# Kernel tuning notes

Hardware: AMD Instinct MI355X
Metric: run time of the kernel (lower is better)

The kernel has to match this reference:

```python
import jax, jax.numpy as jnp
import numpy as np

BLOCK_SIZE = 32
EPS = 1e-6


def setup_inputs() -> dict:
    key = jax.random.key(0)
    k1, k2, k3, k4, k5 = jax.random.split(key, 5)
    B, H, L, D = 2, 16, 4096, 128
    return {
        "query_states": jax.random.normal(k1, (B, H, L, D), dtype=jnp.float32),
        "key_states": jax.random.normal(k2, (B, H, L, D), dtype=jnp.float32),
        "value_states": jax.random.normal(k3, (B, H, L, D), dtype=jnp.float32),
        # learned params; init near torch defaults (ones/zeros) with small noise
        "phi_scale": 1.0 + 0.1 * jax.random.normal(k4, (H, 1, D), dtype=jnp.float32),
        "phi_bias": 0.1 * jax.random.normal(k5, (H, 1, D), dtype=jnp.float32),
    }


def _forward(query_states, key_states, value_states, phi_scale, phi_bias):
    B, H, L, D = query_states.shape
    bs = BLOCK_SIZE
    N = L // bs  # L chosen divisible by block_size (no padding path)

    def feature_map(x):  # x: (B,H,N,bs,D)
        # phi_scale (H,1,D) -> (H,1,1,D) broadcasts over (B,H,N,bs,D)
        y = jax.nn.elu(x * phi_scale[:, None] + phi_bias[:, None]) + 1.0
        return jnp.clip(y, 0.0, 10.0)

    q = query_states.reshape(B, H, N, bs, D)
    k = key_states.reshape(B, H, N, bs, D)
    v = value_states.reshape(B, H, N, bs, D)

    phi_q = feature_map(q)
    phi_k = feature_map(k)

    # move block axis to front for scan: (N,B,H,bs,D)
    pq = jnp.moveaxis(phi_q, 2, 0)
    pk = jnp.moveaxis(phi_k, 2, 0)
    vb = jnp.moveaxis(v, 2, 0)

    S0 = jnp.zeros((B, H, D, D), dtype=jnp.float32)
    Z0 = jnp.zeros((B, H, D), dtype=jnp.float32)

    def step(carry, inp):
        S, Z = carry
        pq_n, pk_n, v_n = inp  # each (B,H,bs,D)
        # block-causal, bidirectional within block: update state BEFORE output
        S = S + jnp.einsum('bhkd,bhke->bhde', pk_n, v_n)
        Z = Z + pk_n.sum(axis=-2)
        num = jnp.einsum('bhqd,bhde->bhqe', pq_n, S)
        den = jnp.maximum(jnp.einsum('bhqd,bhd->bhq', pq_n, Z), EPS)
        return (S, Z), num / den[..., None]

    _, out_blocks = jax.lax.scan(step, (S0, Z0), (pq, pk, vb))  # (N,B,H,bs,D)
    out = jnp.moveaxis(out_blocks, 0, 2).reshape(B, H, L, D)
    return out


def reference(query_states, key_states, value_states, phi_scale, phi_bias):
    return _forward(query_states, key_states, value_states, phi_scale, phi_bias)
```

## Files before the change

kernel.cpp:

```cpp
#include <hip/hip_runtime.h>
#include <stdint.h>

#define BH 32
#define LSEQ 4096
#define DDIM 128
#define BS 32
#define NBLK 128
#define CHUNKS 16
#define BLK_PER_CHUNK 8
#define STATE_SZ (DDIM*DDIM + DDIM)

typedef __attribute__((ext_vector_type(8))) short bf16x8;
typedef __attribute__((ext_vector_type(4))) float f32x4;

__device__ inline uint16_t f2bf(float f) {
    uint32_t x = __builtin_bit_cast(uint32_t, f);
    x += 0x7fffu + ((x >> 16) & 1u);
    return (uint16_t)(x >> 16);
}
__device__ inline float bflo(uint32_t w){ return __builtin_bit_cast(float, w << 16); }
__device__ inline float bfhi(uint32_t w){ return __builtin_bit_cast(float, w & 0xffff0000u); }

__device__ inline float phi_f(float x, float s, float b) {
    float y = fmaf(x, s, b);
    float pos = fminf(y + 1.0f, 10.0f);
    float neg = __expf(y);
    return (y > 0.0f) ? pos : neg;
}

#define SMEM_BYTES 62080

template<bool PHASE2>
__global__ __launch_bounds__(512, 4) void la_phase(
    const float* __restrict__ Q, const float* __restrict__ K,
    const float* __restrict__ V, const float* __restrict__ scale,
    const float* __restrict__ bias, float* __restrict__ states,
    float* __restrict__ out)
{
    extern __shared__ char smem[];
    uint16_t* S_bfT  = (uint16_t*)smem;
    uint16_t* pk_bf  = (uint16_t*)smem;
    uint16_t* v_bf   = (uint16_t*)(smem + 8704);
    uint16_t* pkT    = (uint16_t*)(smem + 34816);
    uint16_t* pq_bf  = pkT;
    uint16_t* vT     = (uint16_t*)(smem + 45056);
    float* Zl        = (float*)(smem + 55296);
    float* Zpart     = Zl + 128;
    float* den_part  = Zpart + 8*128;
    float* inv_den   = den_part + 32*16;

    const int tid  = threadIdx.x;
    const int bid  = blockIdx.x;
    const int bh   = bid >> 4;
    const int ch   = bid & 15;
    const int lane = tid & 63;
    const int wv   = tid >> 6;
    const int i15  = lane & 15;
    const int q4   = lane >> 4;

    const size_t base = (size_t)bh * LSEQ * DDIM;
    const int h = bh & 15;

    const int sr = tid >> 4;
    const int sc = (tid & 15) * 8;

    float sreg[8], breg[8];
    #pragma unroll
    for (int j = 0; j < 8; ++j) {
        sreg[j] = scale[h*DDIM + sc + j];
        breg[j] = bias[h*DDIM + sc + j];
    }

    f32x4 accS[8];
    float* stbase = states + (size_t)(bh*CHUNKS + ch) * STATE_SZ;

    if (PHASE2) {
        #pragma unroll
        for (int mt = 0; mt < 8; ++mt) {
            #pragma unroll
            for (int r = 0; r < 4; ++r) {
                int d = 16*mt + 4*q4 + r;
                accS[mt][r] = stbase[d*DDIM + 16*wv + i15];
            }
        }
        if (tid < 128) Zl[tid] = stbase[DDIM*DDIM + tid];
    } else {
        #pragma unroll
        for (int mt = 0; mt < 8; ++mt) accS[mt] = (f32x4){0.f,0.f,0.f,0.f};
        if (tid < 128) Zl[tid] = 0.f;
    }
    __syncthreads();

    for (int s = 0; s < BLK_PER_CHUNK; ++s) {
        const int blk = ch * BLK_PER_CHUNK + s;
        const size_t rowoff = base + (size_t)(blk*BS + sr) * DDIM + sc;

        {
            const float4 k0 = *(const float4*)(K + rowoff);
            const float4 k1 = *(const float4*)(K + rowoff + 4);
            const float4 v0 = *(const float4*)(V + rowoff);
            const float4 v1 = *(const float4*)(V + rowoff + 4);
            float kp[8] = {k0.x,k0.y,k0.z,k0.w,k1.x,k1.y,k1.z,k1.w};
            float vp[8] = {v0.x,v0.y,v0.z,v0.w,v1.x,v1.y,v1.z,v1.w};
            uint32_t pk[4], pv[4];
            #pragma unroll
            for (int j = 0; j < 4; ++j) {
                uint32_t lo = f2bf(phi_f(kp[2*j],   sreg[2*j],   breg[2*j]));
                uint32_t hi = f2bf(phi_f(kp[2*j+1], sreg[2*j+1], breg[2*j+1]));
                pk[j] = lo | (hi << 16);
                lo = f2bf(vp[2*j]); hi = f2bf(vp[2*j+1]);
                pv[j] = lo | (hi << 16);
            }
            *(uint4*)&pk_bf[sr*136 + sc] = *(uint4*)pk;
            *(uint4*)&v_bf [sr*136 + sc] = *(uint4*)pv;
        }
        __syncthreads();

        {
            const int dp  = tid & 63;
            const int seg = tid >> 6;
            const int r0  = seg * 4;
            uint32_t w0 = *(const uint32_t*)&pk_bf[(r0+0)*136 + 2*dp];
            uint32_t w1 = *(const uint32_t*)&pk_bf[(r0+1)*136 + 2*dp];
            uint32_t w2 = *(const uint32_t*)&pk_bf[(r0+2)*136 + 2*dp];
            uint32_t w3 = *(const uint32_t*)&pk_bf[(r0+3)*136 + 2*dp];
            uint2 lo, hi;
            lo.x = (w0 & 0xffffu) | (w1 << 16);
            lo.y = (w2 & 0xffffu) | (w3 << 16);
            hi.x = (w0 >> 16) | (w1 & 0xffff0000u);
            hi.y = (w2 >> 16) | (w3 & 0xffff0000u);
            *(uint2*)&pkT[(2*dp+0)*40 + r0] = lo;
            *(uint2*)&pkT[(2*dp+1)*40 + r0] = hi;
            Zpart[seg*128 + 2*dp+0] = bflo(w0)+bflo(w1)+bflo(w2)+bflo(w3);
            Zpart[seg*128 + 2*dp+1] = bfhi(w0)+bfhi(w1)+bfhi(w2)+bfhi(w3);
            w0 = *(const uint32_t*)&v_bf[(r0+0)*136 + 2*dp];
            w1 = *(const uint32_t*)&v_bf[(r0+1)*136 + 2*dp];
            w2 = *(const uint32_t*)&v_bf[(r0+2)*136 + 2*dp];
            w3 = *(const uint32_t*)&v_bf[(r0+3)*136 + 2*dp];
            lo.x = (w0 & 0xffffu) | (w1 << 16);
            lo.y = (w2 & 0xffffu) | (w3 << 16);
            hi.x = (w0 >> 16) | (w1 & 0xffff0000u);
            hi.y = (w2 >> 16) | (w3 & 0xffff0000u);
            *(uint2*)&vT[(2*dp+0)*40 + r0] = lo;
            *(uint2*)&vT[(2*dp+1)*40 + r0] = hi;
        }
        __syncthreads();

        if (tid < 128) {
            float z = Zl[tid];
            #pragma unroll
            for (int g = 0; g < 8; ++g) z += Zpart[g*128 + tid];
            Zl[tid] = z;
        }
        {
            bf16x8 bv = *(const bf16x8*)&vT[(16*wv + i15)*40 + 8*q4];
            #pragma unroll
            for (int mt = 0; mt < 8; ++mt) {
                bf16x8 av = *(const bf16x8*)&pkT[(16*mt + i15)*40 + 8*q4];
                accS[mt] = __builtin_amdgcn_mfma_f32_16x16x32_bf16(av, bv, accS[mt], 0, 0, 0);
            }
        }

        if (PHASE2) {
            __syncthreads();

            {
                const float4 a0 = *(const float4*)(Q + rowoff);
                const float4 a1 = *(const float4*)(Q + rowoff + 4);
                float qp[8] = {a0.x,a0.y,a0.z,a0.w,a1.x,a1.y,a1.z,a1.w};
                uint32_t pq[4];
                #pragma unroll
                for (int j = 0; j < 4; ++j) {
                    uint32_t lo = f2bf(phi_f(qp[2*j],   sreg[2*j],   breg[2*j]));
                    uint32_t hi = f2bf(phi_f(qp[2*j+1], sreg[2*j+1], breg[2*j+1]));
                    pq[j] = lo | (hi << 16);
                }
                *(uint4*)&pq_bf[sr*136 + sc] = *(uint4*)pq;
            }
            #pragma unroll
            for (int mt = 0; mt < 8; ++mt) {
                uint2 o;
                o.x = (uint32_t)f2bf(accS[mt][0]) | ((uint32_t)f2bf(accS[mt][1]) << 16);
                o.y = (uint32_t)f2bf(accS[mt][2]) | ((uint32_t)f2bf(accS[mt][3]) << 16);
                *(uint2*)&S_bfT[(16*wv + i15)*136 + 16*mt + 4*q4] = o;
            }
            __syncthreads();

            f32x4 acc2[2];
            acc2[0] = (f32x4){0.f,0.f,0.f,0.f};
            acc2[1] = (f32x4){0.f,0.f,0.f,0.f};
            #pragma unroll
            for (int ks = 0; ks < 4; ++ks) {
                bf16x8 sb = *(const bf16x8*)&S_bfT[(16*wv + i15)*136 + 32*ks + 8*q4];
                #pragma unroll
                for (int qt = 0; qt < 2; ++qt) {
                    bf16x8 qa = *(const bf16x8*)&pq_bf[(16*qt + i15)*136 + 32*ks + 8*q4];
                    acc2[qt] = __builtin_amdgcn_mfma_f32_16x16x32_bf16(qa, sb, acc2[qt], 0, 0, 0);
                }
            }
            {
                const int dq = tid >> 4;
                const int pt = tid & 15;
                float sden = 0.f;
                #pragma unroll
                for (int j = 0; j < 4; ++j) {
                    uint32_t w = *(const uint32_t*)&pq_bf[dq*136 + 8*pt + 2*j];
                    sden += bflo(w) * Zl[8*pt + 2*j] + bfhi(w) * Zl[8*pt + 2*j + 1];
                }
                den_part[dq*16 + pt] = sden;
            }
            __syncthreads();
            if (tid < 32) {
                float sden = 0.f;
                #pragma unroll
                for (int j = 0; j < 16; ++j) sden += den_part[tid*16 + j];
                inv_den[tid] = 1.0f / fmaxf(sden, 1e-6f);
            }
            __syncthreads();

            #pragma unroll
            for (int qt = 0; qt < 2; ++qt) {
                #pragma unroll
                for (int r = 0; r < 4; ++r) {
                    int qrow = 16*qt + 4*q4 + r;
                    float o = acc2[qt][r] * inv_den[qrow];
                    out[base + (size_t)(blk*BS + qrow)*DDIM + 16*wv + i15] = o;
                }
            }
        }
    }

    if (!PHASE2) {
        #pragma unroll
        for (int mt = 0; mt < 8; ++mt) {
            #pragma unroll
            for (int r = 0; r < 4; ++r) {
                int d = 16*mt + 4*q4 + r;
                stbase[d*DDIM + 16*wv + i15] = accS[mt][r];
            }
        }
        if (tid < 128) stbase[DDIM*DDIM + tid] = Zl[tid];
    }
}

__global__ void la_prefix(float* __restrict__ states) {
    const int bh = blockIdx.x >> 4;
    const int sl = blockIdx.x & 15;
    const int slice = STATE_SZ / 16;
    float* p0 = states + (size_t)bh * CHUNKS * STATE_SZ + sl * slice;
    for (int i = threadIdx.x; i < slice; i += 256) {
        float run = 0.f;
        float* p = p0 + i;
        #pragma unroll
        for (int c = 0; c < CHUNKS; ++c) {
            float v = p[(size_t)c * STATE_SZ];
            p[(size_t)c * STATE_SZ] = run;
            run += v;
        }
    }
}

extern "C" void kernel_launch(void* const* d_in, const int* in_sizes, int n_in,
                              void* d_out, int out_size, void* d_ws, size_t ws_size,
                              hipStream_t stream) {
    const float* Q     = (const float*)d_in[0];
    const float* K     = (const float*)d_in[1];
    const float* V     = (const float*)d_in[2];
    const float* scale = (const float*)d_in[3];
    const float* bias  = (const float*)d_in[4];
    float* out    = (float*)d_out;
    float* states = (float*)d_ws;

    hipLaunchKernelGGL((la_phase<false>), dim3(BH*CHUNKS), dim3(512), SMEM_BYTES, stream,
                       Q, K, V, scale, bias, states, out);
    hipLaunchKernelGGL(la_prefix, dim3(BH*16), dim3(256), 0, stream, states);
    hipLaunchKernelGGL((la_phase<true>), dim3(BH*CHUNKS), dim3(512), SMEM_BYTES, stream,
                       Q, K, V, scale, bias, states, out);
}
```

Before: 269.5 us.

## Pipeline chunk loop with register prefetch, shuffle transpose, and swizzled LDS

Restructures the per-chunk loop so the next block's K/V/Q loads are issued into registers while the current block's MFMAs run. The pk/v transpose moves from an LDS round-trip to wave shuffles, LDS tiles get XOR-style swizzles against bank conflicts, and the denominator reduction uses shuffles instead of a shared partial array. Several barriers per iteration are removed, and output stores are deferred by one iteration. The state save/load is made coalesced, and the prefix-sum kernel runs one thread per element with all loads hoisted. The cost is higher register pressure and more complex index logic.

```diff
diff --git a/kernel.cpp b/kernel.cpp
--- a/kernel.cpp
+++ b/kernel.cpp
@@ -1,22 +1,21 @@
 #include <hip/hip_runtime.h>
 #include <stdint.h>
 
-#define BH 32
-#define LSEQ 4096
-#define DDIM 128
-#define BS 32
-#define NBLK 128
 #define CHUNKS 16
-#define BLK_PER_CHUNK 8
-#define STATE_SZ (DDIM*DDIM + DDIM)
+#define STATE_SZ 16512
+#define SMEM_BYTES 64384
 
 typedef __attribute__((ext_vector_type(8))) short bf16x8;
+typedef __attribute__((ext_vector_type(4))) short bf16x4;
 typedef __attribute__((ext_vector_type(4))) float f32x4;
 
 __device__ inline uint16_t f2bf(float f) {
     uint32_t x = __builtin_bit_cast(uint32_t, f);
     x += 0x7fffu + ((x >> 16) & 1u);
     return (uint16_t)(x >> 16);
+}
+__device__ inline uint32_t pack2(float a, float b) {
+    return (uint32_t)f2bf(a) | ((uint32_t)f2bf(b) << 16);
 }
 __device__ inline float bflo(uint32_t w){ return __builtin_bit_cast(float, w << 16); }
 __device__ inline float bfhi(uint32_t w){ return __builtin_bit_cast(float, w & 0xffff0000u); }
@@ -28,7 +27,55 @@
     return (y > 0.0f) ? pos : neg;
 }
 
-#define SMEM_BYTES 62080
+__device__ inline void ld8(float* d, const float* p) {
+    float4 a = *(const float4*)p;
+    float4 b = *(const float4*)(p + 4);
+    d[0]=a.x; d[1]=a.y; d[2]=a.z; d[3]=a.w;
+    d[4]=b.x; d[5]=b.y; d[6]=b.z; d[7]=b.w;
+}
+
+__device__ inline void xpose4(uint32_t p0, uint32_t p1, uint32_t p2, uint32_t p3,
+                              int lane, uint2& lo, uint2& hi, float& z0, float& z1) {
+    const int sb = lane >> 2;
+    const int e0 = lane & 1, e1 = lane & 2;
+    uint32_t w[4];
+    #pragma unroll
+    for (int j = 0; j < 4; ++j) {
+        int src = 16*j + sb;
+        uint32_t t0 = (uint32_t)__shfl((int)p0, src, 64);
+        uint32_t t1 = (uint32_t)__shfl((int)p1, src, 64);
+        uint32_t t2 = (uint32_t)__shfl((int)p2, src, 64);
+        uint32_t t3 = (uint32_t)__shfl((int)p3, src, 64);
+        uint32_t a = e0 ? t1 : t0;
+        uint32_t b = e0 ? t3 : t2;
+        w[j] = e1 ? b : a;
+    }
+    lo.x = (w[0] & 0xffffu) | (w[1] << 16);
+    lo.y = (w[2] & 0xffffu) | (w[3] << 16);
+    hi.x = (w[0] >> 16) | (w[1] & 0xffff0000u);
+    hi.y = (w[2] >> 16) | (w[3] & 0xffff0000u);
+    z0 = bflo(w[0]) + bflo(w[1]) + bflo(w[2]) + bflo(w[3]);
+    z1 = bfhi(w[0]) + bfhi(w[1]) + bfhi(w[2]) + bfhi(w[3]);
+}
+
+__device__ inline bf16x8 fragT(const uint16_t* T, int row, int q4) {
+    const int key = row >> 3;
+    const bf16x4 lo = *(const bf16x4*)&T[row*36 + 4*((2*q4     + key) & 7)];
+    const bf16x4 hi = *(const bf16x4*)&T[row*36 + 4*((2*q4 + 1 + key) & 7)];
+    bf16x8 r;
+    r[0]=lo[0]; r[1]=lo[1]; r[2]=lo[2]; r[3]=lo[3];
+    r[4]=hi[0]; r[5]=hi[1]; r[6]=hi[2]; r[7]=hi[3];
+    return r;
+}
+
+__device__ inline void xpose_store(uint16_t* T, uint32_t p0, uint32_t p1, uint32_t p2,
+                                   uint32_t p3, int lane, int slot8, float* zp, int wv) {
+    uint2 lo, hi; float z0, z1;
+    xpose4(p0, p1, p2, p3, lane, lo, hi, z0, z1);
+    *(uint2*)&T[(2*lane)*36   + 4*slot8] = lo;
+    *(uint2*)&T[(2*lane+1)*36 + 4*slot8] = hi;
+    if (zp) { zp[wv*128 + 2*lane] = z0; zp[wv*128 + 2*lane + 1] = z1; }
+}
 
 template<bool PHASE2>
 __global__ __launch_bounds__(512, 4) void la_phase(
@@ -38,226 +85,226 @@
     float* __restrict__ out)
 {
     extern __shared__ char smem[];
-    uint16_t* S_bfT  = (uint16_t*)smem;
-    uint16_t* pk_bf  = (uint16_t*)smem;
-    uint16_t* v_bf   = (uint16_t*)(smem + 8704);
-    uint16_t* pkT    = (uint16_t*)(smem + 34816);
-    uint16_t* pq_bf  = pkT;
-    uint16_t* vT     = (uint16_t*)(smem + 45056);
-    float* Zl        = (float*)(smem + 55296);
-    float* Zpart     = Zl + 128;
-    float* den_part  = Zpart + 8*128;
-    float* inv_den   = den_part + 32*16;
+    uint16_t* pkT     = (uint16_t*)(smem);
+    uint16_t* vT      = (uint16_t*)(smem + 9216);
+    uint16_t* S_bfT   = (uint16_t*)(smem + 18432);
+    uint16_t* pq_bf   = (uint16_t*)(smem + 51200);
+    float*    Zpart   = (float*)(smem + 59648);
+    float*    Zl      = (float*)(smem + 63744);
+    float*    inv_den = (float*)(smem + 64256);
 
     const int tid  = threadIdx.x;
-    const int bid  = blockIdx.x;
-    const int bh   = bid >> 4;
-    const int ch   = bid & 15;
+    const int bh   = blockIdx.x >> 4;
+    const int ch   = blockIdx.x & 15;
     const int lane = tid & 63;
     const int wv   = tid >> 6;
     const int i15  = lane & 15;
     const int q4   = lane >> 4;
-
-    const size_t base = (size_t)bh * LSEQ * DDIM;
+    const int sr   = tid >> 4;
+    const int sc   = (tid & 15) * 8;
+    const int slot8 = (wv + (lane >> 2)) & 7;
+
+    const size_t base = (size_t)bh * 4096 * 128;
     const int h = bh & 15;
-
-    const int sr = tid >> 4;
-    const int sc = (tid & 15) * 8;
 
     float sreg[8], breg[8];
     #pragma unroll
     for (int j = 0; j < 8; ++j) {
-        sreg[j] = scale[h*DDIM + sc + j];
-        breg[j] = bias[h*DDIM + sc + j];
-    }
+        sreg[j] = scale[h*128 + sc + j];
+        breg[j] = bias[h*128 + sc + j];
+    }
+
+    float* stb = states + (size_t)(bh*CHUNKS + ch) * STATE_SZ;
 
     f32x4 accS[8];
-    float* stbase = states + (size_t)(bh*CHUNKS + ch) * STATE_SZ;
-
     if (PHASE2) {
         #pragma unroll
         for (int mt = 0; mt < 8; ++mt) {
-            #pragma unroll
-            for (int r = 0; r < 4; ++r) {
-                int d = 16*mt + 4*q4 + r;
-                accS[mt][r] = stbase[d*DDIM + 16*wv + i15];
-            }
-        }
-        if (tid < 128) Zl[tid] = stbase[DDIM*DDIM + tid];
+            float4 t = *(const float4*)(stb + wv*2048 + mt*256 + lane*4);
+            accS[mt] = (f32x4){t.x, t.y, t.z, t.w};
+        }
+        if (tid < 128) Zl[tid] = stb[16384 + tid];
     } else {
         #pragma unroll
-        for (int mt = 0; mt < 8; ++mt) accS[mt] = (f32x4){0.f,0.f,0.f,0.f};
+        for (int mt = 0; mt < 8; ++mt) accS[mt] = (f32x4){0.f, 0.f, 0.f, 0.f};
         if (tid < 128) Zl[tid] = 0.f;
     }
+
+    float kr[8], vr[8], qr[8], fq[8];
+    {
+        const size_t ro = base + (size_t)((ch*8)*32 + sr) * 128 + sc;
+        ld8(kr, K + ro);
+        ld8(vr, V + ro);
+        if (PHASE2) ld8(qr, Q + ro);
+    }
+    {
+        uint32_t pk0 = pack2(phi_f(kr[0],sreg[0],breg[0]), phi_f(kr[1],sreg[1],breg[1]));
+        uint32_t pk1 = pack2(phi_f(kr[2],sreg[2],breg[2]), phi_f(kr[3],sreg[3],breg[3]));
+        uint32_t pk2 = pack2(phi_f(kr[4],sreg[4],breg[4]), phi_f(kr[5],sreg[5],breg[5]));
+        uint32_t pk3 = pack2(phi_f(kr[6],sreg[6],breg[6]), phi_f(kr[7],sreg[7],breg[7]));
+        xpose_store(pkT, pk0, pk1, pk2, pk3, lane, slot8, Zpart, wv);
+        uint32_t pv0 = pack2(vr[0], vr[1]);
+        uint32_t pv1 = pack2(vr[2], vr[3]);
+        uint32_t pv2 = pack2(vr[4], vr[5]);
+        uint32_t pv3 = pack2(vr[6], vr[7]);
+        xpose_store(vT, pv0, pv1, pv2, pv3, lane, slot8, (float*)0, wv);
+    }
+    if (PHASE2) {
+        uint32_t hq[4];
+        #pragma unroll
+        for (int j = 0; j < 4; ++j) {
+            hq[j] = pack2(phi_f(qr[2*j],   sreg[2*j],   breg[2*j]),
+                          phi_f(qr[2*j+1], sreg[2*j+1], breg[2*j+1]));
+            fq[2*j]   = bflo(hq[j]);
+            fq[2*j+1] = bfhi(hq[j]);
+        }
+        *(uint2*)&pq_bf[sr*132 + sc]     = (uint2){hq[0], hq[1]};
+        *(uint2*)&pq_bf[sr*132 + sc + 4] = (uint2){hq[2], hq[3]};
+    }
     __syncthreads();
 
-    for (int s = 0; s < BLK_PER_CHUNK; ++s) {
-        const int blk = ch * BLK_PER_CHUNK + s;
-        const size_t rowoff = base + (size_t)(blk*BS + sr) * DDIM + sc;
-
+    float o8[8];
+    #pragma unroll 1
+    for (int i = 0; i < 8; ++i) {
+        if (PHASE2 && i > 0) {
+            uint32_t hq[4];
+            #pragma unroll
+            for (int j = 0; j < 4; ++j) {
+                hq[j] = pack2(phi_f(qr[2*j],   sreg[2*j],   breg[2*j]),
+                              phi_f(qr[2*j+1], sreg[2*j+1], breg[2*j+1]));
+                fq[2*j]   = bflo(hq[j]);
+                fq[2*j+1] = bfhi(hq[j]);
+            }
+            *(uint2*)&pq_bf[sr*132 + sc]     = (uint2){hq[0], hq[1]};
+            *(uint2*)&pq_bf[sr*132 + sc + 4] = (uint2){hq[2], hq[3]};
+        }
+        if (i < 7) {
+            const size_t ro = base + (size_t)((ch*8 + i + 1)*32 + sr) * 128 + sc;
+            ld8(kr, K + ro);
+            ld8(vr, V + ro);
+            if (PHASE2) ld8(qr, Q + ro);
+        }
         {
-            const float4 k0 = *(const float4*)(K + rowoff);
-            const float4 k1 = *(const float4*)(K + rowoff + 4);
-            const float4 v0 = *(const float4*)(V + rowoff);
-            const float4 v1 = *(const float4*)(V + rowoff + 4);
-            float kp[8] = {k0.x,k0.y,k0.z,k0.w,k1.x,k1.y,k1.z,k1.w};
-            float vp[8] = {v0.x,v0.y,v0.z,v0.w,v1.x,v1.y,v1.z,v1.w};
-            uint32_t pk[4], pv[4];
-            #pragma unroll
-            for (int j = 0; j < 4; ++j) {
-                uint32_t lo = f2bf(phi_f(kp[2*j],   sreg[2*j],   breg[2*j]));
-                uint32_t hi = f2bf(phi_f(kp[2*j+1], sreg[2*j+1], breg[2*j+1]));
-                pk[j] = lo | (hi << 16);
-                lo = f2bf(vp[2*j]); hi = f2bf(vp[2*j+1]);
-                pv[j] = lo | (hi << 16);
-            }
-            *(uint4*)&pk_bf[sr*136 + sc] = *(uint4*)pk;
-            *(uint4*)&v_bf [sr*136 + sc] = *(uint4*)pv;
-        }
-        __syncthreads();
-
-        {
-            const int dp  = tid & 63;
-            const int seg = tid >> 6;
-            const int r0  = seg * 4;
-            uint32_t w0 = *(const uint32_t*)&pk_bf[(r0+0)*136 + 2*dp];
-            uint32_t w1 = *(const uint32_t*)&pk_bf[(r0+1)*136 + 2*dp];
-            uint32_t w2 = *(const uint32_t*)&pk_bf[(r0+2)*136 + 2*dp];
-            uint32_t w3 = *(const uint32_t*)&pk_bf[(r0+3)*136 + 2*dp];
-            uint2 lo, hi;
-            lo.x = (w0 & 0xffffu) | (w1 << 16);
-            lo.y = (w2 & 0xffffu) | (w3 << 16);
-            hi.x = (w0 >> 16) | (w1 & 0xffff0000u);
-            hi.y = (w2 >> 16) | (w3 & 0xffff0000u);
-            *(uint2*)&pkT[(2*dp+0)*40 + r0] = lo;
-            *(uint2*)&pkT[(2*dp+1)*40 + r0] = hi;
-            Zpart[seg*128 + 2*dp+0] = bflo(w0)+bflo(w1)+bflo(w2)+bflo(w3);
-            Zpart[seg*128 + 2*dp+1] = bfhi(w0)+bfhi(w1)+bfhi(w2)+bfhi(w3);
-            w0 = *(const uint32_t*)&v_bf[(r0+0)*136 + 2*dp];
-            w1 = *(const uint32_t*)&v_bf[(r0+1)*136 + 2*dp];
-            w2 = *(const uint32_t*)&v_bf[(r0+2)*136 + 2*dp];
-            w3 = *(const uint32_t*)&v_bf[(r0+3)*136 + 2*dp];
-            lo.x = (w0 & 0xffffu) | (w1 << 16);
-            lo.y = (w2 & 0xffffu) | (w3 << 16);
-            hi.x = (w0 >> 16) | (w1 & 0xffff0000u);
-            hi.y = (w2 >> 16) | (w3 & 0xffff0000u);
-            *(uint2*)&vT[(2*dp+0)*40 + r0] = lo;
-            *(uint2*)&vT[(2*dp+1)*40 + r0] = hi;
-        }
-        __syncthreads();
-
+            bf16x8 bv = fragT(vT, 16*wv + i15, q4);
+            #pragma unroll
+            for (int mt = 0; mt < 8; ++mt) {
+                bf16x8 av = fragT(pkT, 16*mt + i15, q4);
+                accS[mt] = __builtin_amdgcn_mfma_f32_16x16x32_bf16(av, bv, accS[mt], 0, 0, 0);
+            }
+        }
         if (tid < 128) {
             float z = Zl[tid];
             #pragma unroll
             for (int g = 0; g < 8; ++g) z += Zpart[g*128 + tid];
             Zl[tid] = z;
         }
-        {
-            bf16x8 bv = *(const bf16x8*)&vT[(16*wv + i15)*40 + 8*q4];
-            #pragma unroll
-            for (int mt = 0; mt < 8; ++mt) {
-                bf16x8 av = *(const bf16x8*)&pkT[(16*mt + i15)*40 + 8*q4];
-                accS[mt] = __builtin_amdgcn_mfma_f32_16x16x32_bf16(av, bv, accS[mt], 0, 0, 0);
-            }
-        }
-
         if (PHASE2) {
-            __syncthreads();
-
-            {
-                const float4 a0 = *(const float4*)(Q + rowoff);
-                const float4 a1 = *(const float4*)(Q + rowoff + 4);
-                float qp[8] = {a0.x,a0.y,a0.z,a0.w,a1.x,a1.y,a1.z,a1.w};
-                uint32_t pq[4];
-                #pragma unroll
-                for (int j = 0; j < 4; ++j) {
-                    uint32_t lo = f2bf(phi_f(qp[2*j],   sreg[2*j],   breg[2*j]));
-                    uint32_t hi = f2bf(phi_f(qp[2*j+1], sreg[2*j+1], breg[2*j+1]));
-                    pq[j] = lo | (hi << 16);
-                }
-                *(uint4*)&pq_bf[sr*136 + sc] = *(uint4*)pq;
-            }
+            const int e = 16*wv + i15;
             #pragma unroll
             for (int mt = 0; mt < 8; ++mt) {
                 uint2 o;
-                o.x = (uint32_t)f2bf(accS[mt][0]) | ((uint32_t)f2bf(accS[mt][1]) << 16);
-                o.y = (uint32_t)f2bf(accS[mt][2]) | ((uint32_t)f2bf(accS[mt][3]) << 16);
-                *(uint2*)&S_bfT[(16*wv + i15)*136 + 16*mt + 4*q4] = o;
-            }
-            __syncthreads();
-
+                o.x = pack2(accS[mt][0], accS[mt][1]);
+                o.y = pack2(accS[mt][2], accS[mt][3]);
+                const int ps = (4*mt + q4 + e) & 31;
+                *(uint2*)&S_bfT[e*128 + 4*ps] = o;
+            }
+            if (i > 0) {
+                const int blk = ch*8 + i - 1;
+                #pragma unroll
+                for (int qt = 0; qt < 2; ++qt)
+                #pragma unroll
+                for (int r = 0; r < 4; ++r) {
+                    const int qrow = 16*qt + 4*q4 + r;
+                    out[base + (size_t)(blk*32 + qrow)*128 + 16*wv + i15] =
+                        o8[qt*4 + r] * inv_den[qrow];
+                }
+            }
+        }
+        __syncthreads();
+        if (PHASE2) {
             f32x4 acc2[2];
-            acc2[0] = (f32x4){0.f,0.f,0.f,0.f};
-            acc2[1] = (f32x4){0.f,0.f,0.f,0.f};
+            acc2[0] = (f32x4){0.f, 0.f, 0.f, 0.f};
+            acc2[1] = (f32x4){0.f, 0.f, 0.f, 0.f};
+            const int eb = 16*wv + i15;
             #pragma unroll
             for (int ks = 0; ks < 4; ++ks) {
-                bf16x8 sb = *(const bf16x8*)&S_bfT[(16*wv + i15)*136 + 32*ks + 8*q4];
+                const int p0 = (8*ks + 2*q4 + eb) & 31;
+                const bf16x4 slo = *(const bf16x4*)&S_bfT[eb*128 + 4*p0];
+                const bf16x4 shi = *(const bf16x4*)&S_bfT[eb*128 + 4*((p0 + 1) & 31)];
+                bf16x8 sb;
+                sb[0]=slo[0]; sb[1]=slo[1]; sb[2]=slo[2]; sb[3]=slo[3];
+                sb[4]=shi[0]; sb[5]=shi[1]; sb[6]=shi[2]; sb[7]=shi[3];
                 #pragma unroll
                 for (int qt = 0; qt < 2; ++qt) {
-                    bf16x8 qa = *(const bf16x8*)&pq_bf[(16*qt + i15)*136 + 32*ks + 8*q4];
+                    const int qr0 = 16*qt + i15;
+                    const bf16x4 qlo = *(const bf16x4*)&pq_bf[qr0*132 + 32*ks + 8*q4];
+                    const bf16x4 qhi = *(const bf16x4*)&pq_bf[qr0*132 + 32*ks + 8*q4 + 4];
+                    bf16x8 qa;
+                    qa[0]=qlo[0]; qa[1]=qlo[1]; qa[2]=qlo[2]; qa[3]=qlo[3];
+                    qa[4]=qhi[0]; qa[5]=qhi[1]; qa[6]=qhi[2]; qa[7]=qhi[3];
                     acc2[qt] = __builtin_amdgcn_mfma_f32_16x16x32_bf16(qa, sb, acc2[qt], 0, 0, 0);
                 }
             }
-            {
-                const int dq = tid >> 4;
-                const int pt = tid & 15;
-                float sden = 0.f;
-                #pragma unroll
-                for (int j = 0; j < 4; ++j) {
-                    uint32_t w = *(const uint32_t*)&pq_bf[dq*136 + 8*pt + 2*j];
-                    sden += bflo(w) * Zl[8*pt + 2*j] + bfhi(w) * Zl[8*pt + 2*j + 1];
-                }
-                den_part[dq*16 + pt] = sden;
-            }
-            __syncthreads();
-            if (tid < 32) {
-                float sden = 0.f;
-                #pragma unroll
-                for (int j = 0; j < 16; ++j) sden += den_part[tid*16 + j];
-                inv_den[tid] = 1.0f / fmaxf(sden, 1e-6f);
-            }
-            __syncthreads();
-
-            #pragma unroll
-            for (int qt = 0; qt < 2; ++qt) {
-                #pragma unroll
-                for (int r = 0; r < 4; ++r) {
-                    int qrow = 16*qt + 4*q4 + r;
-                    float o = acc2[qt][r] * inv_den[qrow];
-                    out[base + (size_t)(blk*BS + qrow)*DDIM + 16*wv + i15] = o;
-                }
-            }
-        }
-    }
-
-    if (!PHASE2) {
+            float4 za = *(const float4*)&Zl[sc];
+            float4 zb = *(const float4*)&Zl[sc + 4];
+            float sden = fq[0]*za.x + fq[1]*za.y + fq[2]*za.z + fq[3]*za.w
+                       + fq[4]*zb.x + fq[5]*zb.y + fq[6]*zb.z + fq[7]*zb.w;
+            sden += __shfl_xor(sden, 1, 64);
+            sden += __shfl_xor(sden, 2, 64);
+            sden += __shfl_xor(sden, 4, 64);
+            sden += __shfl_xor(sden, 8, 64);
+            if ((tid & 15) == 0) inv_den[sr] = 1.0f / fmaxf(sden, 1e-6f);
+            #pragma unroll
+            for (int qt = 0; qt < 2; ++qt)
+            #pragma unroll
+            for (int r = 0; r < 4; ++r) o8[qt*4 + r] = acc2[qt][r];
+        }
+        if (i < 7) {
+            uint32_t pk0 = pack2(phi_f(kr[0],sreg[0],breg[0]), phi_f(kr[1],sreg[1],breg[1]));
+            uint32_t pk1 = pack2(phi_f(kr[2],sreg[2],breg[2]), phi_f(kr[3],sreg[3],breg[3]));
+            uint32_t pk2 = pack2(phi_f(kr[4],sreg[4],breg[4]), phi_f(kr[5],sreg[5],breg[5]));
+            uint32_t pk3 = pack2(phi_f(kr[6],sreg[6],breg[6]), phi_f(kr[7],sreg[7],breg[7]));
+            xpose_store(pkT, pk0, pk1, pk2, pk3, lane, slot8, Zpart, wv);
+            uint32_t pv0 = pack2(vr[0], vr[1]);
+            uint32_t pv1 = pack2(vr[2], vr[3]);
+            uint32_t pv2 = pack2(vr[4], vr[5]);
+            uint32_t pv3 = pack2(vr[6], vr[7]);
+            xpose_store(vT, pv0, pv1, pv2, pv3, lane, slot8, (float*)0, wv);
+        }
+        __syncthreads();
+    }
+
+    if (PHASE2) {
+        const int blk = ch*8 + 7;
+        #pragma unroll
+        for (int qt = 0; qt < 2; ++qt)
+        #pragma unroll
+        for (int r = 0; r < 4; ++r) {
+            const int qrow = 16*qt + 4*q4 + r;
+            out[base + (size_t)(blk*32 + qrow)*128 + 16*wv + i15] =
+                o8[qt*4 + r] * inv_den[qrow];
+        }
+    } else {
         #pragma unroll
         for (int mt = 0; mt < 8; ++mt) {
-            #pragma unroll
-            for (int r = 0; r < 4; ++r) {
-                int d = 16*mt + 4*q4 + r;
-                stbase[d*DDIM + 16*wv + i15] = accS[mt][r];
-            }
-        }
-        if (tid < 128) stbase[DDIM*DDIM + tid] = Zl[tid];
-    }
-}
-
-__global__ void la_prefix(float* __restrict__ states) {
-    const int bh = blockIdx.x >> 4;
-    const int sl = blockIdx.x & 15;
-    const int slice = STATE_SZ / 16;
-    float* p0 = states + (size_t)bh * CHUNKS * STATE_SZ + sl * slice;
-    for (int i = threadIdx.x; i < slice; i += 256) {
-        float run = 0.f;
-        float* p = p0 + i;
-        #pragma unroll
-        for (int c = 0; c < CHUNKS; ++c) {
-            float v = p[(size_t)c * STATE_SZ];
-            p[(size_t)c * STATE_SZ] = run;
-            run += v;
-        }
-    }
+            float4 t = {accS[mt][0], accS[mt][1], accS[mt][2], accS[mt][3]};
+            *(float4*)(stb + wv*2048 + mt*256 + lane*4) = t;
+        }
+        if (tid < 128) stb[16384 + tid] = Zl[tid];
+    }
+}
+
+__global__ __launch_bounds__(256) void la_prefix(float* __restrict__ states) {
+    const int gid = blockIdx.x * 256 + threadIdx.x;
+    const int bh  = gid / STATE_SZ;
+    const int e   = gid - bh * STATE_SZ;
+    float* p = states + (size_t)bh * CHUNKS * STATE_SZ + e;
+    float v[CHUNKS];
+    #pragma unroll
+    for (int c = 0; c < CHUNKS; ++c) v[c] = p[c * STATE_SZ];
+    float run = 0.f;
+    #pragma unroll
+    for (int c = 0; c < CHUNKS; ++c) { p[c * STATE_SZ] = run; run += v[c]; }
 }
 
 extern "C" void kernel_launch(void* const* d_in, const int* in_sizes, int n_in,
@@ -271,9 +318,9 @@
     float* out    = (float*)d_out;
     float* states = (float*)d_ws;
 
-    hipLaunchKernelGGL((la_phase<false>), dim3(BH*CHUNKS), dim3(512), SMEM_BYTES, stream,
+    hipLaunchKernelGGL((la_phase<false>), dim3(512), dim3(512), SMEM_BYTES, stream,
                        Q, K, V, scale, bias, states, out);
-    hipLaunchKernelGGL(la_prefix, dim3(BH*16), dim3(256), 0, stream, states);
-    hipLaunchKernelGGL((la_phase<true>), dim3(BH*CHUNKS), dim3(512), SMEM_BYTES, stream,
+    hipLaunchKernelGGL(la_prefix, dim3((32*STATE_SZ)/256), dim3(256), 0, stream, states);
+    hipLaunchKernelGGL((la_phase<true>), dim3(512), dim3(512), SMEM_BYTES, stream,
                        Q, K, V, scale, bias, states, out);
 }
```

After: 321.5 us. +19.3%, slower.
